# Optimization experiments

Hardware: AMD Instinct MI355X
Metric: run time of the kernel (lower is better)

The kernel has to match this reference:

```python
import jax, jax.numpy as jnp
import numpy as np

N, E, T, B = 20000, 400000, 1500000, 128
H, INT, BAS, OUT_EMB, OUT = 128, 64, 8, 256, 1
NR, SBF_DIM = 6, 42  # num_radial, num_spherical*num_radial
L, NBS, NAS, NOUT = 4, 1, 2, 3  # layers, before-skip, after-skip, output lins


def _w(key, shape, scale=0.1):
    return jax.random.normal(key, shape, dtype=jnp.float32) * scale


def setup_inputs() -> dict:
    key = jax.random.key(0)
    ks = iter(jax.random.split(key, 64))
    inp = {}
    inp['x'] = jax.random.normal(next(ks), (N, 48), dtype=jnp.float32)
    inp['edge_attr'] = jax.random.normal(next(ks), (E, 12), dtype=jnp.float32)
    inp['rbf'] = jax.random.normal(next(ks), (E, NR), dtype=jnp.float32)
    inp['sbf'] = jax.random.normal(next(ks), (T, SBF_DIM), dtype=jnp.float32)
    inp['i'] = jax.random.randint(next(ks), (E,), 0, N)
    inp['idx_kj'] = jax.random.randint(next(ks), (T,), 0, E)
    inp['idx_ji'] = jax.random.randint(next(ks), (T,), 0, E)
    inp['batch'] = jnp.sort(jax.random.randint(next(ks), (N,), 0, B))
    # input projections
    inp['W_node'] = _w(next(ks), (48, H))
    inp['W_edge'] = _w(next(ks), (12, H))
    # update_e params, stacked over layers
    inp['We_rbf1'] = _w(next(ks), (L, NR, BAS))
    inp['We_rbf2'] = _w(next(ks), (L, BAS, H))
    inp['We_sbf1'] = _w(next(ks), (L, SBF_DIM, BAS))
    inp['We_sbf2'] = _w(next(ks), (L, BAS, INT))
    inp['We_rbf'] = _w(next(ks), (L, NR, H))
    inp['We_kj'] = _w(next(ks), (L, H, H)); inp['be_kj'] = _w(next(ks), (L, H))
    inp['We_ji'] = _w(next(ks), (L, H, H)); inp['be_ji'] = _w(next(ks), (L, H))
    inp['We_down'] = _w(next(ks), (L, H, INT))
    inp['We_up'] = _w(next(ks), (L, INT, H))
    inp['We_cat'] = _w(next(ks), (L, H, H))
    inp['Wres_before'] = _w(next(ks), (L, NBS, 2, H, H)); inp['bres_before'] = _w(next(ks), (L, NBS, 2, H))
    inp['We_lin'] = _w(next(ks), (L, H, H)); inp['be_lin'] = _w(next(ks), (L, H))
    inp['Wres_after'] = _w(next(ks), (L, NAS, 2, H, H)); inp['bres_after'] = _w(next(ks), (L, NAS, 2, H))
    # update_v params, stacked over layers
    inp['Wv_up'] = _w(next(ks), (L, H, OUT_EMB)); inp['bv_up'] = _w(next(ks), (L, OUT_EMB))
    inp['Wv_lins'] = _w(next(ks), (L, NOUT, OUT_EMB, OUT_EMB)); inp['bv_lins'] = _w(next(ks), (L, NOUT, OUT_EMB))
    inp['Wv_out'] = _w(next(ks), (L, OUT_EMB, OUT))
    return inp


def _forward(x, edge_attr, rbf, sbf, W_node, W_edge, We_rbf1, We_rbf2, We_sbf1,
             We_sbf2, We_rbf, We_kj, be_kj, We_ji, be_ji, We_down, We_up, We_cat,
             Wres_before, bres_before, We_lin, be_lin, Wres_after, bres_after,
             Wv_up, bv_up, Wv_lins, bv_lins, Wv_out, i, idx_kj, idx_ji, batch):
    silu = jax.nn.silu  # swish
    seg = lambda v, idx, n: jax.ops.segment_sum(v, idx, num_segments=n)

    e1 = edge_attr @ W_edge            # [E, H]  (init edge state; init_e unused in source fwd)
    v = x @ W_node                     # [N, H]
    u = seg(v, batch, B)               # [B, H] -> init_u(zeros, v, batch)

    # precompute sbf projection per layer inside loop (depends on layer weights)
    for l in range(L):
        # ---- update_e ----
        x_ji = silu(e1 @ We_ji[l] + be_ji[l])
        x_kj = silu(e1 @ We_kj[l] + be_kj[l])
        r = (rbf @ We_rbf1[l]) @ We_rbf2[l]          # [E, H]
        x_kj = silu((x_kj * r) @ We_down[l])          # [E, INT]
        s = (sbf @ We_sbf1[l]) @ We_sbf2[l]           # [T, INT]
        m = x_kj[idx_kj] * s                          # gather to triplets
        agg = seg(m, idx_ji, E)                       # scatter back to edges
        x_kj = silu(agg @ We_up[l])                   # [E, H]
        e = silu((x_ji + x_kj) @ We_cat[l])
        for r_ in range(NBS):
            e = e + silu(silu(e @ Wres_before[l, r_, 0] + bres_before[l, r_, 0]) @ Wres_before[l, r_, 1] + bres_before[l, r_, 1])
        e = silu(e @ We_lin[l] + be_lin[l]) + e1
        for r_ in range(NAS):
            e = e + silu(silu(e @ Wres_after[l, r_, 0] + bres_after[l, r_, 0]) @ Wres_after[l, r_, 1] + bres_after[l, r_, 1])
        e1 = e
        e2 = (rbf @ We_rbf[l]) * e1                   # [E, H]
        # ---- update_v ----
        vn = seg(e2, i, N)                            # [N, H]
        vn = vn @ Wv_up[l] + bv_up[l]                 # [N, OUT_EMB]
        for k in range(NOUT):
            vn = silu(vn @ Wv_lins[l, k] + bv_lins[l, k])
        vn = vn @ Wv_out[l]                           # [N, OUT]
        # ---- update_u ----
        u = u + seg(vn, batch, B) if l > 0 else seg(vn, batch, B)
        if l == 0:
            # first update_u adds onto u (which held init [B,H]); but shapes differ
            # in source only because out is added to u of same shape. Here init u
            # is [B,H] from v=lin_node(x) and vn is [B,OUT]; the source's init_u
            # uses v=[N,H] so u=[B,H] then adds v=[N,OUT] scatters -> in torch this
            # broadcasts only if OUT==H. Faithful behavior with OUT=1: broadcast add.
            pass
        # (handled above via broadcasting in jnp if needed)
    return u


def reference(x, edge_attr, rbf, sbf, W_node, W_edge, We_rbf1, We_rbf2, We_sbf1,
              We_sbf2, We_rbf, We_kj, be_kj, We_ji, be_ji, We_down, We_up, We_cat,
              Wres_before, bres_before, We_lin, be_lin, Wres_after, bres_after,
              Wv_up, bv_up, Wv_lins, bv_lins, Wv_out, i, idx_kj, idx_ji, batch):
    silu = jax.nn.silu
    seg = lambda v, idx, n: jax.ops.segment_sum(v, idx, num_segments=n)

    e1 = edge_attr @ W_edge
    v = x @ W_node
    u = seg(v, batch, B)  # [B, H]
    for l in range(L):
        x_ji = silu(e1 @ We_ji[l] + be_ji[l])
        x_kj = silu(e1 @ We_kj[l] + be_kj[l])
        r = (rbf @ We_rbf1[l]) @ We_rbf2[l]
        x_kj = silu((x_kj * r) @ We_down[l])
        s = (sbf @ We_sbf1[l]) @ We_sbf2[l]
        agg = seg(x_kj[idx_kj] * s, idx_ji, E)
        x_kj = silu(agg @ We_up[l])
        e = silu((x_ji + x_kj) @ We_cat[l])
        for r_ in range(NBS):
            e = e + silu(silu(e @ Wres_before[l, r_, 0] + bres_before[l, r_, 0]) @ Wres_before[l, r_, 1] + bres_before[l, r_, 1])
        e = silu(e @ We_lin[l] + be_lin[l]) + e1
        for r_ in range(NAS):
            e = e + silu(silu(e @ Wres_after[l, r_, 0] + bres_after[l, r_, 0]) @ Wres_after[l, r_, 1] + bres_after[l, r_, 1])
        e1 = e
        e2 = (rbf @ We_rbf[l]) * e1
        vn = seg(e2, i, N) @ Wv_up[l] + bv_up[l]
        for k in range(NOUT):
            vn = silu(vn @ Wv_lins[l, k] + bv_lins[l, k])
        vn = vn @ Wv_out[l]              # [N, 1]
        u = u + seg(vn, batch, B)        # broadcast [B,1] onto [B,H]
    return u
```

## Files before the change

kernel.cpp:

```cpp
#include <hip/hip_runtime.h>
#include <hip/hip_bf16.h>
#include <cstddef>

#define NN 20000
#define EE 400000
#define TT 1500000
#define BB 128
#define HH 128
#define INTD 64
#define OUT_EMB 256
#define SBF_DIM 42
#define NRAD 6

#define SA_C 136

typedef __attribute__((ext_vector_type(8))) short bf16x8;
typedef __attribute__((ext_vector_type(4))) float f32x4;

__device__ __forceinline__ float silu_f(float v) {
    return v / (1.0f + __expf(-v));
}
__device__ __forceinline__ unsigned short f2b(float f) {
    __hip_bfloat16 h = __float2bfloat16(f);
    unsigned short u; __builtin_memcpy(&u, &h, 2); return u;
}
__device__ __forceinline__ float b2f(unsigned short u) {
    __hip_bfloat16 h; __builtin_memcpy(&h, &u, 2); return __bfloat162float(h);
}

template <int NU4>
__device__ __forceinline__ void loadWlin(uint4 (&rg)[NU4], const unsigned short* W, int tid) {
#pragma unroll
    for (int j = 0; j < NU4; ++j) rg[j] = *(const uint4*)(W + ((size_t)tid + j * 512) * 8);
}
template <int NU4, int SEGS>
__device__ __forceinline__ void storeWs(const uint4 (&rg)[NU4], unsigned short* Ws, int tid) {
#pragma unroll
    for (int j = 0; j < NU4; ++j) {
        int i = tid + j * 512;
        int n = i / SEGS, seg = i % SEGS;
        *(uint4*)&Ws[n * SA_C + seg * 8] = rg[j];
    }
}

__device__ __forceinline__ void st4(unsigned short* Cs, int m, int f0, const float* v) {
    ushort4 u = make_ushort4(f2b(v[0]), f2b(v[1]), f2b(v[2]), f2b(v[3]));
    *(ushort4*)&Cs[m * SA_C + f0] = u;
}

template <int KCNT>
__device__ __forceinline__ void mfma_f(const unsigned short* Cs, const unsigned short* Ws,
                                       int lm, int quad, int fw0, int ew0, f32x4 acc[2][4]) {
#pragma unroll
    for (int kc = 0; kc < KCNT; ++kc) {
        bf16x8 wf[2], xf[4];
#pragma unroll
        for (int mi = 0; mi < 2; ++mi)
            wf[mi] = *(const bf16x8*)&Ws[(fw0 + mi * 16 + lm) * SA_C + kc * 32 + quad * 8];
#pragma unroll
        for (int ni = 0; ni < 4; ++ni)
            xf[ni] = *(const bf16x8*)&Cs[(ew0 + ni * 16 + lm) * SA_C + kc * 32 + quad * 8];
#pragma unroll
        for (int mi = 0; mi < 2; ++mi)
#pragma unroll
            for (int ni = 0; ni < 4; ++ni)
                acc[mi][ni] = __builtin_amdgcn_mfma_f32_16x16x32_bf16(wf[mi], xf[ni], acc[mi][ni], 0, 0, 0);
    }
}

template <int KCNT>
__device__ __forceinline__ void mfma_d2(const unsigned short* Cs, const unsigned short* Ws,
                                        int lm, int quad, int fw0, int ew0, f32x4 acc[2][2]) {
#pragma unroll
    for (int kc = 0; kc < KCNT; ++kc) {
        bf16x8 wf[2], xf[2];
#pragma unroll
        for (int mi = 0; mi < 2; ++mi)
            wf[mi] = *(const bf16x8*)&Ws[(fw0 + mi * 16 + lm) * SA_C + kc * 32 + quad * 8];
#pragma unroll
        for (int ni = 0; ni < 2; ++ni)
            xf[ni] = *(const bf16x8*)&Cs[(ew0 + ni * 16 + lm) * SA_C + kc * 32 + quad * 8];
#pragma unroll
        for (int mi = 0; mi < 2; ++mi)
#pragma unroll
            for (int ni = 0; ni < 2; ++ni)
                acc[mi][ni] = __builtin_amdgcn_mfma_f32_16x16x32_bf16(wf[mi], xf[ni], acc[mi][ni], 0, 0, 0);
    }
}

__global__ __launch_bounds__(512, 2)
void mk1(const unsigned short* __restrict__ e1b,
         const unsigned short* __restrict__ w_ji, const unsigned short* __restrict__ w_kj,
         const unsigned short* __restrict__ w_down,
         const float* __restrict__ be_ji, const float* __restrict__ be_kj,
         const float* __restrict__ rbf, const float* __restrict__ Crbf_l,
         unsigned short* __restrict__ buf1, unsigned short* __restrict__ bufC) {
    __shared__ unsigned short Cs[128 * SA_C];
    __shared__ unsigned short Ws[128 * SA_C];
    __shared__ float rbfS[128 * 6];
    __shared__ float CrbfS[768];

    const int tid = threadIdx.x;
    const size_t row0 = (size_t)blockIdx.x * 128;
    const int lane = tid & 63, wave = tid >> 6, lm = lane & 15, quad = lane >> 4;
    const int rw0 = (wave >> 1) * 32;
    const int cw0 = (wave & 1) * 64;
    const int fw0d = (wave & 1) * 32;
    const int ew0d = (wave >> 1) * 32;

    uint4 wreg[4]; uint4 wregd[2];

    for (int i = tid; i < 2048; i += 512) {
        int r = i >> 4, seg = i & 15;
        *(uint4*)&Cs[r * SA_C + seg * 8] = *(const uint4*)(e1b + (row0 + r) * 128 + seg * 8);
    }
    loadWlin<4>(wreg, w_ji, tid); storeWs<4, 16>(wreg, Ws, tid);
    for (int i = tid; i < 768; i += 512) { rbfS[i] = rbf[row0 * 6 + i]; CrbfS[i] = Crbf_l[i]; }
    __syncthreads();

    f32x4 jreg[2][4], acc[2][4];
#pragma unroll
    for (int mi = 0; mi < 2; ++mi)
#pragma unroll
        for (int ni = 0; ni < 4; ++ni) jreg[mi][ni] = (f32x4){0.f, 0.f, 0.f, 0.f};
    loadWlin<4>(wreg, w_kj, tid);
    mfma_f<4>(Cs, Ws, lm, quad, rw0, cw0, jreg);
    __syncthreads();
    storeWs<4, 16>(wreg, Ws, tid);
    __syncthreads();

#pragma unroll
    for (int mi = 0; mi < 2; ++mi)
#pragma unroll
        for (int ni = 0; ni < 4; ++ni) acc[mi][ni] = (f32x4){0.f, 0.f, 0.f, 0.f};
    loadWlin<2>(wregd, w_down, tid);
    mfma_f<4>(Cs, Ws, lm, quad, rw0, cw0, acc);
    __syncthreads();
#pragma unroll
    for (int mi = 0; mi < 2; ++mi) {
        const int f0 = rw0 + mi * 16 + quad * 4;
        const float4 bb = *(const float4*)(be_kj + f0);
#pragma unroll
        for (int ni = 0; ni < 4; ++ni) {
            const int m = cw0 + ni * 16 + lm;
            float4 rv = {0.f, 0.f, 0.f, 0.f};
#pragma unroll
            for (int j = 0; j < 6; ++j) {
                float rb = rbfS[m * 6 + j];
                float4 c4 = *(const float4*)&CrbfS[j * 128 + f0];
                rv.x += rb * c4.x; rv.y += rb * c4.y; rv.z += rb * c4.z; rv.w += rb * c4.w;
            }
            float v4[4];
#pragma unroll
            for (int r = 0; r < 4; ++r) {
                float v = silu_f(acc[mi][ni][r] + (&bb.x)[r]);
                v4[r] = b2f(f2b(v)) * (&rv.x)[r];
            }
            st4(Cs, m, f0, v4);
        }
    }
    storeWs<2, 16>(wregd, Ws, tid);
    __syncthreads();

    f32x4 accd[2][2];
#pragma unroll
    for (int mi = 0; mi < 2; ++mi)
#pragma unroll
        for (int ni = 0; ni < 2; ++ni) accd[mi][ni] = (f32x4){0.f, 0.f, 0.f, 0.f};
    mfma_d2<4>(Cs, Ws, lm, quad, fw0d, ew0d, accd);
    __syncthreads();
#pragma unroll
    for (int mi = 0; mi < 2; ++mi) {
        const int f0 = fw0d + mi * 16 + quad * 4;
#pragma unroll
        for (int ni = 0; ni < 2; ++ni) {
            const int m = ew0d + ni * 16 + lm;
            float v4[4];
#pragma unroll
            for (int r = 0; r < 4; ++r) v4[r] = silu_f(accd[mi][ni][r]);
            st4(Cs, m, f0, v4);
        }
    }
    __syncthreads();
    for (int i = tid; i < 1024; i += 512) {
        int r = i >> 3, seg = i & 7;
        *(uint4*)(bufC + (row0 + r) * 64 + seg * 8) = *(const uint4*)&Cs[r * SA_C + seg * 8];
    }
    __syncthreads();
#pragma unroll
    for (int mi = 0; mi < 2; ++mi) {
        const int f0 = rw0 + mi * 16 + quad * 4;
        const float4 bj = *(const float4*)(be_ji + f0);
#pragma unroll
        for (int ni = 0; ni < 4; ++ni) {
            const int m = cw0 + ni * 16 + lm;
            float v4[4];
#pragma unroll
            for (int r = 0; r < 4; ++r) v4[r] = silu_f(jreg[mi][ni][r] + (&bj.x)[r]);
            st4(Cs, m, f0, v4);
        }
    }
    __syncthreads();
    for (int i = tid; i < 2048; i += 512) {
        int r = i >> 4, seg = i & 15;
        *(uint4*)(buf1 + (row0 + r) * 128 + seg * 8) = *(const uint4*)&Cs[r * SA_C + seg * 8];
    }
}

__global__ __launch_bounds__(512, 2)
void mk2(const unsigned short* __restrict__ bufD, const unsigned short* __restrict__ buf1g,
         float* __restrict__ e1f, unsigned short* __restrict__ e1b,
         const unsigned short* __restrict__ w_up, const unsigned short* __restrict__ w_cat,
         const unsigned short* __restrict__ w_rb0, const unsigned short* __restrict__ w_rb1,
         const unsigned short* __restrict__ w_lin,
         const unsigned short* __restrict__ w_ra0, const unsigned short* __restrict__ w_ra1,
         const unsigned short* __restrict__ w_ra2, const unsigned short* __restrict__ w_ra3,
         const float* __restrict__ b_rb0, const float* __restrict__ b_rb1,
         const float* __restrict__ b_lin,
         const float* __restrict__ b_ra0, const float* __restrict__ b_ra1,
         const float* __restrict__ b_ra2, const float* __restrict__ b_ra3) {
    __shared__ unsigned short Cs[128 * SA_C];
    __shared__ unsigned short Ws[128 * SA_C];

    const int tid = threadIdx.x;
    const size_t row0 = (size_t)blockIdx.x * 128;
    const int lane = tid & 63, wave = tid >> 6, lm = lane & 15, quad = lane >> 4;
    const int rw0 = (wave >> 1) * 32, cw0 = (wave & 1) * 64;

    f32x4 acc[2][4], state[2][4];
    uint4 wreg[4];

#define ZERO_ACC()                                                 \
    _Pragma("unroll") for (int mi = 0; mi < 2; ++mi)               \
    _Pragma("unroll") for (int ni = 0; ni < 4; ++ni)               \
        acc[mi][ni] = (f32x4){0.f, 0.f, 0.f, 0.f};

#define TILE_LOOP(PRELOAD, BODY, POST)                          \
    _Pragma("unroll") for (int mi = 0; mi < 2; ++mi) {          \
      const int f0 = rw0 + mi * 16 + quad * 4;                  \
      _Pragma("unroll") for (int ni = 0; ni < 4; ++ni) {        \
        const int m = cw0 + ni * 16 + lm;                       \
        const size_t goff = (size_t)(row0 + m) * 128 + f0;      \
        (void)goff;                                             \
        PRELOAD                                                 \
        float v4[4];                                            \
        _Pragma("unroll") for (int r = 0; r < 4; ++r) { BODY }  \
        st4(Cs, m, f0, v4);                                     \
        POST } }

    for (int i = tid; i < 1024; i += 512) {
        int r = i >> 3, seg = i & 7;
        *(uint4*)&Cs[r * SA_C + seg * 8] = *(const uint4*)(bufD + (row0 + r) * 64 + seg * 8);
    }
    {
        uint4 wu[2];
        loadWlin<2>(wu, w_up, tid); storeWs<2, 8>(wu, Ws, tid);
    }
    __syncthreads();

    ZERO_ACC()
    loadWlin<4>(wreg, w_cat, tid);
    mfma_f<2>(Cs, Ws, lm, quad, rw0, cw0, acc);
    __syncthreads();
    TILE_LOOP(
        ushort4 xj = *(const ushort4*)(buf1g + goff);,
        { float v = silu_f(acc[mi][ni][r]);
          v4[r] = b2f((&xj.x)[r]) + b2f(f2b(v)); },
    )
    storeWs<4, 16>(wreg, Ws, tid);
    __syncthreads();

#define PHASE_HEAD(WNEXT)                          \
    ZERO_ACC()                                     \
    loadWlin<4>(wreg, (WNEXT), tid);               \
    mfma_f<4>(Cs, Ws, lm, quad, rw0, cw0, acc);    \
    __syncthreads();

#define PHASE_TAIL()                               \
    storeWs<4, 16>(wreg, Ws, tid);                 \
    __syncthreads();

    PHASE_HEAD(w_rb0)
    TILE_LOOP(,
        { float v = silu_f(acc[mi][ni][r]); state[mi][ni][r] = v; v4[r] = v; },
    )
    PHASE_TAIL()

    PHASE_HEAD(w_rb1)
    TILE_LOOP(
        float4 b4 = *(const float4*)(b_rb0 + f0);,
        { v4[r] = silu_f(acc[mi][ni][r] + (&b4.x)[r]); },
    )
    PHASE_TAIL()

    PHASE_HEAD(w_lin)
    TILE_LOOP(
        float4 b4 = *(const float4*)(b_rb1 + f0);,
        { float v = state[mi][ni][r] + silu_f(acc[mi][ni][r] + (&b4.x)[r]);
          state[mi][ni][r] = v; v4[r] = v; },
    )
    PHASE_TAIL()

    PHASE_HEAD(w_ra0)
    TILE_LOOP(
        float4 b4 = *(const float4*)(b_lin + f0);
        float4 e4 = *(const float4*)(e1f + goff);,
        { float v = silu_f(acc[mi][ni][r] + (&b4.x)[r]) + (&e4.x)[r];
          state[mi][ni][r] = v; v4[r] = v; },
    )
    PHASE_TAIL()

    PHASE_HEAD(w_ra1)
    TILE_LOOP(
        float4 b4 = *(const float4*)(b_ra0 + f0);,
        { v4[r] = silu_f(acc[mi][ni][r] + (&b4.x)[r]); },
    )
    PHASE_TAIL()

    PHASE_HEAD(w_ra2)
    TILE_LOOP(
        float4 b4 = *(const float4*)(b_ra1 + f0);,
        { float v = state[mi][ni][r] + silu_f(acc[mi][ni][r] + (&b4.x)[r]);
          state[mi][ni][r] = v; v4[r] = v; },
    )
    PHASE_TAIL()

    PHASE_HEAD(w_ra3)
    TILE_LOOP(
        float4 b4 = *(const float4*)(b_ra2 + f0);,
        { v4[r] = silu_f(acc[mi][ni][r] + (&b4.x)[r]); },
    )
    PHASE_TAIL()

    ZERO_ACC()
    mfma_f<4>(Cs, Ws, lm, quad, rw0, cw0, acc);
    __syncthreads();
    TILE_LOOP(
        float4 b4 = *(const float4*)(b_ra3 + f0);,
        { float v = state[mi][ni][r] + silu_f(acc[mi][ni][r] + (&b4.x)[r]);
          state[mi][ni][r] = v; v4[r] = v; },
        { float4 ev; ev.x = v4[0]; ev.y = v4[1]; ev.z = v4[2]; ev.w = v4[3];
          *(float4*)(e1f + goff) = ev; }
    )
    __syncthreads();
    for (int i = tid; i < 2048; i += 512) {
        int r = i >> 4, seg = i & 15;
        *(uint4*)(e1b + (row0 + r) * 128 + seg * 8) = *(const uint4*)&Cs[r * SA_C + seg * 8];
    }
#undef PHASE_HEAD
#undef PHASE_TAIL
#undef TILE_LOOP
#undef ZERO_ACC
}

__global__ void transpose_w(const float* __restrict__ src, unsigned short* __restrict__ dst,
                            int B, int K, int N) {
    size_t total = (size_t)B * K * N;
    size_t i = (size_t)blockIdx.x * 256 + threadIdx.x;
    if (i >= total) return;
    int b = i / ((size_t)K * N);
    size_t rem = i - (size_t)b * K * N;
    int k = rem / N, n = rem % N;
    dst[(size_t)b * K * N + (size_t)n * K + k] = f2b(src[i]);
}

template <int K>
__launch_bounds__(256)
__global__ void gemm_k(const float* __restrict__ A, const float* __restrict__ W,
                       const float* __restrict__ bias, float* __restrict__ out,
                       unsigned short* __restrict__ outb, int N, int act) {
    constexpr int KC = (K <= 128) ? K : 128;
    __shared__ float As[32][KC + 1];
    __shared__ float Ws[KC * 64];
    const int tid = threadIdx.x;
    const size_t row0 = (size_t)blockIdx.x * 32;
    const int tx = tid & 15, ty = tid >> 4;
    const int c0 = tx * 4, r0 = ty * 2;

    for (int nc0 = 0; nc0 < N; nc0 += 64) {
        float acc[2][4] = {{0.f, 0.f, 0.f, 0.f}, {0.f, 0.f, 0.f, 0.f}};
        for (int kc0 = 0; kc0 < K; kc0 += KC) {
            __syncthreads();
            for (int idx = tid; idx < 32 * KC / 4; idx += 256) {
                int r = idx / (KC / 4);
                int kk = (idx % (KC / 4)) * 4;
                float4 v = *(const float4*)(A + (row0 + r) * K + kc0 + kk);
                As[r][kk] = v.x; As[r][kk + 1] = v.y;
                As[r][kk + 2] = v.z; As[r][kk + 3] = v.w;
            }
            for (int idx = tid; idx < KC * 16; idx += 256) {
                int k = idx >> 4;
                int cc = (idx & 15) * 4;
                *(float4*)&Ws[k * 64 + cc] =
                    *(const float4*)(W + (size_t)(kc0 + k) * N + nc0 + cc);
            }
            __syncthreads();
#pragma unroll 4
            for (int k = 0; k < KC; ++k) {
                float a0 = As[r0][k], a1 = As[r0 + 1][k];
                float4 w = *(const float4*)&Ws[k * 64 + c0];
                acc[0][0] += a0 * w.x; acc[0][1] += a0 * w.y;
                acc[0][2] += a0 * w.z; acc[0][3] += a0 * w.w;
                acc[1][0] += a1 * w.x; acc[1][1] += a1 * w.y;
                acc[1][2] += a1 * w.z; acc[1][3] += a1 * w.w;
            }
        }
#pragma unroll
        for (int i = 0; i < 2; ++i) {
            size_t off = (row0 + r0 + i) * N + nc0 + c0;
            float4 v = make_float4(acc[i][0], acc[i][1], acc[i][2], acc[i][3]);
            if (bias) {
                float4 b = *(const float4*)(bias + nc0 + c0);
                v.x += b.x; v.y += b.y; v.z += b.z; v.w += b.w;
            }
            if (act) {
                v.x = silu_f(v.x); v.y = silu_f(v.y);
                v.z = silu_f(v.z); v.w = silu_f(v.w);
            }
            if (out) *(float4*)(out + off) = v;
            if (outb) {
                ushort4 u = make_ushort4(f2b(v.x), f2b(v.y), f2b(v.z), f2b(v.w));
                *(ushort4*)(outb + off) = u;
            }
        }
    }
}

__global__ void combine_rbf(const float* __restrict__ W1, const float* __restrict__ W2,
                            float* __restrict__ C) {
    int l = blockIdx.x;
    const float* w1 = W1 + l * 48;
    const float* w2 = W2 + l * 1024;
    float* c = C + l * 768;
    for (int idx = threadIdx.x; idx < 768; idx += 256) {
        int j = idx >> 7, h = idx & 127;
        float s = 0.f;
#pragma unroll
        for (int p = 0; p < 8; ++p) s += w1[j * 8 + p] * w2[p * 128 + h];
        c[idx] = s;
    }
}

__global__ void hist_kernel(const int* __restrict__ idx, int n, int* __restrict__ cnt) {
    int t = blockIdx.x * 256 + threadIdx.x;
    if (t < n) atomicAdd(&cnt[idx[t]], 1);
}

__launch_bounds__(1024)
__global__ void scan1(const int* __restrict__ cnt, int n, int* __restrict__ offs,
                      int* __restrict__ partials) {
    __shared__ int tmp[1024];
    int tid = threadIdx.x;
    int i = blockIdx.x * 1024 + tid;
    int v = (i < n) ? cnt[i] : 0;
    tmp[tid] = v; __syncthreads();
    for (int d = 1; d < 1024; d <<= 1) {
        int t = (tid >= d) ? tmp[tid - d] : 0; __syncthreads();
        tmp[tid] += t; __syncthreads();
    }
    if (i < n) offs[i] = tmp[tid] - v;
    if (tid == 1023) partials[blockIdx.x] = tmp[1023];
}

__launch_bounds__(1024)
__global__ void scan2(int* __restrict__ partials, int nb, int n, int* __restrict__ offs) {
    __shared__ int tmp[1024];
    int tid = threadIdx.x;
    int v = (tid < nb) ? partials[tid] : 0;
    tmp[tid] = v; __syncthreads();
    for (int d = 1; d < 1024; d <<= 1) {
        int t = (tid >= d) ? tmp[tid - d] : 0; __syncthreads();
        tmp[tid] += t; __syncthreads();
    }
    if (tid < nb) partials[tid] = tmp[tid] - v;
    if (tid == 1023) offs[n] = tmp[1023];
}

__launch_bounds__(1024)
__global__ void scan3(int n, int* __restrict__ offs, const int* __restrict__ partials,
                      int* __restrict__ cur) {
    int i = blockIdx.x * 1024 + threadIdx.x;
    if (i < n) { int o = offs[i] + partials[blockIdx.x]; offs[i] = o; cur[i] = o; }
}

__global__ void fill_kernel(const int* __restrict__ idx, int n,
                            int* __restrict__ cur, int* __restrict__ lst) {
    int t = blockIdx.x * 256 + threadIdx.x;
    if (t < n) {
        int p = atomicAdd(&cur[idx[t]], 1);
        lst[p] = t;
    }
}

__launch_bounds__(128)
__global__ void p8_kernel(const float* __restrict__ sbf, const float* __restrict__ W1,
                          float* __restrict__ p8) {
    __shared__ float S[128 * 43];
    __shared__ float Wl[SBF_DIM * 8];
    int tid = threadIdx.x;
    for (int i = tid; i < SBF_DIM * 8; i += 128) Wl[i] = W1[i];
    size_t base = (size_t)blockIdx.x * 128;
    int rows = (TT - base) < 128 ? (int)(TT - base) : 128;
    const float* src = sbf + base * SBF_DIM;
    for (int i = tid; i < rows * SBF_DIM; i += 128) {
        int r = i / SBF_DIM, j = i - r * SBF_DIM;
        S[r * 43 + j] = src[i];
    }
    __syncthreads();
    if (tid >= rows) return;
    float pv[8] = {0.f, 0.f, 0.f, 0.f, 0.f, 0.f, 0.f, 0.f};
    for (int j = 0; j < SBF_DIM; ++j) {
        float sv = S[tid * 43 + j];
#pragma unroll
        for (int p = 0; p < 8; ++p) pv[p] += sv * Wl[j * 8 + p];
    }
    float4* o = (float4*)(p8 + (base + tid) * 8);
    o[0] = make_float4(pv[0], pv[1], pv[2], pv[3]);
    o[1] = make_float4(pv[4], pv[5], pv[6], pv[7]);
}

__launch_bounds__(256)
__global__ void triplet_gather(const float* __restrict__ p8, const float* __restrict__ W2,
                               const unsigned short* __restrict__ xkj,
                               const int* __restrict__ idx_kj,
                               const int* __restrict__ offsT, const int* __restrict__ tlist,
                               unsigned short* __restrict__ agg) {
    int lane = threadIdx.x & 63;
    int wv = threadIdx.x >> 6;
    int e = blockIdx.x * 4 + wv;
    if (e >= EE) return;
    float w2c[8];
#pragma unroll
    for (int p = 0; p < 8; ++p) w2c[p] = W2[p * INTD + lane];
    int b = offsT[e], en = offsT[e + 1];
    float acc = 0.f;
    for (int q = b; q < en; ++q) {
        int t = tlist[q];
        int k = idx_kj[t];
        const float4* pr = (const float4*)(p8 + (size_t)t * 8);
        float4 p0 = pr[0], p1 = pr[1];
        float s = p0.x * w2c[0] + p0.y * w2c[1] + p0.z * w2c[2] + p0.w * w2c[3]
                + p1.x * w2c[4] + p1.y * w2c[5] + p1.z * w2c[6] + p1.w * w2c[7];
        acc += s * b2f(xkj[(size_t)k * INTD + lane]);
    }
    agg[(size_t)e * INTD + lane] = f2b(acc);
}

__launch_bounds__(256)
__global__ void e2_gather(const float* __restrict__ rbf, const float* __restrict__ Wr,
                          const float* __restrict__ e1f, const int* __restrict__ offsE,
                          const int* __restrict__ elist, float* __restrict__ vseg) {
    int h = threadIdx.x & 127;
    int sub = threadIdx.x >> 7;
    int n = blockIdx.x * 2 + sub;
    if (n >= NN) return;
    float c0 = Wr[0 * 128 + h], c1 = Wr[1 * 128 + h], c2 = Wr[2 * 128 + h],
          c3 = Wr[3 * 128 + h], c4 = Wr[4 * 128 + h], c5 = Wr[5 * 128 + h];
    int b = offsE[n], en = offsE[n + 1];
    float a0 = 0.f, a1 = 0.f, a2 = 0.f, a3 = 0.f;
    int q = b;
    for (; q + 4 <= en; q += 4) {
        int ea = elist[q], eb = elist[q + 1], ec = elist[q + 2], ed = elist[q + 3];
        const float* ra = rbf + (size_t)ea * NRAD;
        const float* rb = rbf + (size_t)eb * NRAD;
        const float* rc = rbf + (size_t)ec * NRAD;
        const float* rd = rbf + (size_t)ed * NRAD;
        float fa = e1f[(size_t)ea * 128 + h];
        float fb = e1f[(size_t)eb * 128 + h];
        float fc = e1f[(size_t)ec * 128 + h];
        float fd = e1f[(size_t)ed * 128 + h];
        float sa = ra[0] * c0 + ra[1] * c1 + ra[2] * c2 + ra[3] * c3 + ra[4] * c4 + ra[5] * c5;
        float sb = rb[0] * c0 + rb[1] * c1 + rb[2] * c2 + rb[3] * c3 + rb[4] * c4 + rb[5] * c5;
        float sc = rc[0] * c0 + rc[1] * c1 + rc[2] * c2 + rc[3] * c3 + rc[4] * c4 + rc[5] * c5;
        float sd = rd[0] * c0 + rd[1] * c1 + rd[2] * c2 + rd[3] * c3 + rd[4] * c4 + rd[5] * c5;
        a0 += sa * fa; a1 += sb * fb; a2 += sc * fc; a3 += sd * fd;
    }
    for (; q < en; ++q) {
        int e = elist[q];
        const float* rr = rbf + (size_t)e * NRAD;
        float s = rr[0] * c0 + rr[1] * c1 + rr[2] * c2 + rr[3] * c3 + rr[4] * c4 + rr[5] * c5;
        a0 += s * e1f[(size_t)e * 128 + h];
    }
    vseg[(size_t)n * 128 + h] = (a0 + a1) + (a2 + a3);
}

__global__ void scatter_u0(const float* __restrict__ v, const int* __restrict__ batch,
                           float* __restrict__ u0) {
    int idx = blockIdx.x * 256 + threadIdx.x;
    int h = idx & 127;
    int n = idx >> 7;
    atomicAdd(&u0[(size_t)batch[n] * 128 + h], v[idx]);
}

__launch_bounds__(256)
__global__ void vout_scatter(const float* __restrict__ vn, const float* __restrict__ Wv_out,
                             const int* __restrict__ batch, float* __restrict__ sbatch) {
    int wave = threadIdx.x >> 6, lane = threadIdx.x & 63;
    int n = blockIdx.x * 4 + wave;
    if (n >= NN) return;
    const float* row = vn + (size_t)n * OUT_EMB;
    float s = 0.f;
#pragma unroll
    for (int k = lane; k < OUT_EMB; k += 64) s += row[k] * Wv_out[k];
#pragma unroll
    for (int off = 32; off > 0; off >>= 1) s += __shfl_down(s, off);
    if (lane == 0) atomicAdd(&sbatch[batch[n]], s);
}

__global__ void final_out(const float* __restrict__ u0, const float* __restrict__ sb,
                          float* __restrict__ out) {
    int idx = blockIdx.x * 256 + threadIdx.x;
    out[idx] = u0[idx] + sb[idx >> 7];
}

extern "C" void kernel_launch(void* const* d_in, const int* in_sizes, int n_in,
                              void* d_out, int out_size, void* d_ws, size_t ws_size,
                              hipStream_t stream) {
    const float* x         = (const float*)d_in[0];
    const float* edge_attr = (const float*)d_in[1];
    const float* rbf       = (const float*)d_in[2];
    const float* sbf       = (const float*)d_in[3];
    const int*   iidx      = (const int*)d_in[4];
    const int*   idx_kj    = (const int*)d_in[5];
    const int*   idx_ji    = (const int*)d_in[6];
    const int*   batch     = (const int*)d_in[7];
    const float* W_node    = (const float*)d_in[8];
    const float* W_edge    = (const float*)d_in[9];
    const float* We_rbf1   = (const float*)d_in[10];
    const float* We_rbf2   = (const float*)d_in[11];
    const float* We_sbf1   = (const float*)d_in[12];
    const float* We_sbf2   = (const float*)d_in[13];
    const float* We_rbf    = (const float*)d_in[14];
    const float* We_kj     = (const float*)d_in[15];
    const float* be_kj     = (const float*)d_in[16];
    const float* We_ji     = (const float*)d_in[17];
    const float* be_ji     = (const float*)d_in[18];
    const float* We_down   = (const float*)d_in[19];
    const float* We_up     = (const float*)d_in[20];
    const float* We_cat    = (const float*)d_in[21];
    const float* Wres_b    = (const float*)d_in[22];
    const float* bres_b    = (const float*)d_in[23];
    const float* We_lin    = (const float*)d_in[24];
    const float* be_lin    = (const float*)d_in[25];
    const float* Wres_a    = (const float*)d_in[26];
    const float* bres_a    = (const float*)d_in[27];
    const float* Wv_up     = (const float*)d_in[28];
    const float* bv_up     = (const float*)d_in[29];
    const float* Wv_lins   = (const float*)d_in[30];
    const float* bv_lins   = (const float*)d_in[31];
    const float* Wv_out    = (const float*)d_in[32];
    float* out = (float*)d_out;

    unsigned short* e1b  = (unsigned short*)d_ws;
    unsigned short* buf1 = e1b  + (size_t)EE * HH;
    unsigned short* scr2 = buf1 + (size_t)EE * HH;
    unsigned short* bufC = scr2 + (size_t)EE * HH;
    unsigned short* bufD = bufC + (size_t)EE * INTD;
    unsigned short* endu = bufD + (size_t)EE * INTD;
    float* e1f    = (float*)endu;
    float* tail   = e1f + (size_t)EE * HH;
    float* u0     = tail;
    float* sbatch = u0 + BB * HH;
    float* Crbf   = sbatch + 256;
    int*   iptr   = (int*)(Crbf + 4 * 768);
    int* cntT  = iptr;               iptr += EE;
    int* offsT = iptr;               iptr += EE + 1;
    int* curT  = iptr;               iptr += EE;
    int* tlist = iptr;               iptr += TT;
    int* cntE  = iptr;               iptr += NN;
    int* offsE = iptr;               iptr += NN + 1;
    int* curE  = iptr;               iptr += NN;
    int* elist = iptr;               iptr += EE;
    int* partials = iptr;            iptr += 1024;
    unsigned short* wptr = (unsigned short*)iptr;
    unsigned short* wt_ji   = wptr;  wptr += 4 * 16384;
    unsigned short* wt_kj   = wptr;  wptr += 4 * 16384;
    unsigned short* wt_down = wptr;  wptr += 4 * 8192;
    unsigned short* wt_up   = wptr;  wptr += 4 * 8192;
    unsigned short* wt_cat  = wptr;  wptr += 4 * 16384;
    unsigned short* wt_resb = wptr;  wptr += 8 * 16384;
    unsigned short* wt_lin  = wptr;  wptr += 4 * 16384;
    unsigned short* wt_resa = wptr;  wptr += 16 * 16384;
    float* p8 = (float*)scr2;
    float* vseg = (float*)bufC;
    float* vn1  = vseg + (size_t)NN * HH;
    float* vn2  = vn1 + (size_t)NN * OUT_EMB;

    hipMemsetAsync(u0, 0, (size_t)BB * HH * sizeof(float), stream);
    hipMemsetAsync(sbatch, 0, 256 * sizeof(float), stream);
    combine_rbf<<<4, 256, 0, stream>>>(We_rbf1, We_rbf2, Crbf);

    transpose_w<<<(4 * 16384 + 255) / 256, 256, 0, stream>>>(We_ji, wt_ji, 4, 128, 128);
    transpose_w<<<(4 * 16384 + 255) / 256, 256, 0, stream>>>(We_kj, wt_kj, 4, 128, 128);
    transpose_w<<<(4 * 8192 + 255) / 256, 256, 0, stream>>>(We_down, wt_down, 4, 128, 64);
    transpose_w<<<(4 * 8192 + 255) / 256, 256, 0, stream>>>(We_up, wt_up, 4, 64, 128);
    transpose_w<<<(4 * 16384 + 255) / 256, 256, 0, stream>>>(We_cat, wt_cat, 4, 128, 128);
    transpose_w<<<(8 * 16384 + 255) / 256, 256, 0, stream>>>(Wres_b, wt_resb, 8, 128, 128);
    transpose_w<<<(4 * 16384 + 255) / 256, 256, 0, stream>>>(We_lin, wt_lin, 4, 128, 128);
    transpose_w<<<(16 * 16384 + 255) / 256, 256, 0, stream>>>(Wres_a, wt_resa, 16, 128, 128);

    hipMemsetAsync(cntT, 0, EE * sizeof(int), stream);
    hipMemsetAsync(cntE, 0, NN * sizeof(int), stream);
    hist_kernel<<<(TT + 255) / 256, 256, 0, stream>>>(idx_ji, TT, cntT);
    hist_kernel<<<(EE + 255) / 256, 256, 0, stream>>>(iidx, EE, cntE);
    int nbT = (EE + 1023) / 1024, nbE = (NN + 1023) / 1024;
    scan1<<<nbT, 1024, 0, stream>>>(cntT, EE, offsT, partials);
    scan2<<<1, 1024, 0, stream>>>(partials, nbT, EE, offsT);
    scan3<<<nbT, 1024, 0, stream>>>(EE, offsT, partials, curT);
    fill_kernel<<<(TT + 255) / 256, 256, 0, stream>>>(idx_ji, TT, curT, tlist);
    scan1<<<nbE, 1024, 0, stream>>>(cntE, NN, offsE, partials);
    scan2<<<1, 1024, 0, stream>>>(partials, nbE, NN, offsE);
    scan3<<<nbE, 1024, 0, stream>>>(NN, offsE, partials, curE);
    fill_kernel<<<(EE + 255) / 256, 256, 0, stream>>>(iidx, EE, curE, elist);

    gemm_k<12><<<EE / 32, 256, 0, stream>>>(edge_attr, W_edge, nullptr, e1f, e1b, HH, 0);
    gemm_k<48><<<NN / 32, 256, 0, stream>>>(x, W_node, nullptr, vseg, nullptr, HH, 0);
    scatter_u0<<<NN * HH / 256, 256, 0, stream>>>(vseg, batch, u0);

    const int GR = EE / 128;
    for (int l = 0; l < 4; ++l) {
        mk1<<<GR, 512, 0, stream>>>(e1b, wt_ji + l * 16384, wt_kj + l * 16384,
                                    wt_down + l * 8192, be_ji + l * HH, be_kj + l * HH,
                                    rbf, Crbf + l * 768, buf1, bufC);
        p8_kernel<<<(TT + 127) / 128, 128, 0, stream>>>(sbf, We_sbf1 + l * SBF_DIM * 8, p8);
        triplet_gather<<<EE / 4, 256, 0, stream>>>(p8, We_sbf2 + l * 8 * INTD, bufC,
                                                   idx_kj, offsT, tlist, bufD);
        mk2<<<GR, 512, 0, stream>>>(bufD, buf1, e1f, e1b,
            wt_up + l * 8192, wt_cat + l * 16384,
            wt_resb + (l * 2 + 0) * 16384, wt_resb + (l * 2 + 1) * 16384,
            wt_lin + l * 16384,
            wt_resa + ((l * 2 + 0) * 2 + 0) * 16384, wt_resa + ((l * 2 + 0) * 2 + 1) * 16384,
            wt_resa + ((l * 2 + 1) * 2 + 0) * 16384, wt_resa + ((l * 2 + 1) * 2 + 1) * 16384,
            bres_b + (l * 2 + 0) * HH, bres_b + (l * 2 + 1) * HH, be_lin + l * HH,
            bres_a + ((l * 2 + 0) * 2 + 0) * HH, bres_a + ((l * 2 + 0) * 2 + 1) * HH,
            bres_a + ((l * 2 + 1) * 2 + 0) * HH, bres_a + ((l * 2 + 1) * 2 + 1) * HH);
        e2_gather<<<(NN + 1) / 2, 256, 0, stream>>>(rbf, We_rbf + (size_t)l * NRAD * HH,
                                                    e1f, offsE, elist, vseg);
        gemm_k<128><<<NN / 32, 256, 0, stream>>>(vseg, Wv_up + (size_t)l * HH * OUT_EMB,
                                                 bv_up + l * OUT_EMB, vn1, nullptr, OUT_EMB, 0);
        gemm_k<256><<<NN / 32, 256, 0, stream>>>(vn1, Wv_lins + (size_t)(l * 3 + 0) * 65536,
                                                 bv_lins + (l * 3 + 0) * 256, vn2, nullptr, OUT_EMB, 1);
        gemm_k<256><<<NN / 32, 256, 0, stream>>>(vn2, Wv_lins + (size_t)(l * 3 + 1) * 65536,
                                                 bv_lins + (l * 3 + 1) * 256, vn1, nullptr, OUT_EMB, 1);
        gemm_k<256><<<NN / 32, 256, 0, stream>>>(vn1, Wv_lins + (size_t)(l * 3 + 2) * 65536,
                                                 bv_lins + (l * 3 + 2) * 256, vn2, nullptr, OUT_EMB, 1);
        vout_scatter<<<NN / 4, 256, 0, stream>>>(vn2, Wv_out + l * OUT_EMB, batch, sbatch);
    }
    final_out<<<BB * HH / 256, 256, 0, stream>>>(u0, sbatch, out);
}
```

Measured before the change: 6.905 ms.

## Fuse node MLP chain into one bf16 MFMA kernel and stage mk2 output via LDS

Replaces the per-layer chain of four fp32 gemm_k launches plus the vout_scatter reduction with a single mkv kernel. It keeps a 128-row tile in LDS across up-projection, three 256x256 SiLU layers and the output dot product, using bf16 MFMA with pre-transposed weights. This removes the intermediate vn1/vn2 global round trips and the launch overhead. mk2's final epilogue now stages fp32 results in shared memory, so the e1f and e1b stores are fully coalesced and e1b is rounded from full precision. The cost is lower precision in the node MLP (bf16 activations and weights) and a kernel limited to one block per CU by its large LDS footprint.

```diff
diff --git a/kernel.cpp b/kernel.cpp
--- a/kernel.cpp
+++ b/kernel.cpp
@@ -219,8 +219,10 @@
          const float* __restrict__ b_lin,
          const float* __restrict__ b_ra0, const float* __restrict__ b_ra1,
          const float* __restrict__ b_ra2, const float* __restrict__ b_ra3) {
-    __shared__ unsigned short Cs[128 * SA_C];
-    __shared__ unsigned short Ws[128 * SA_C];
+    __shared__ unsigned short SMEM[2 * 128 * SA_C];
+    unsigned short* Cs = SMEM;
+    unsigned short* Ws = SMEM + 128 * SA_C;
+    float* Fs = (float*)SMEM;
 
     const int tid = threadIdx.x;
     const size_t row0 = (size_t)blockIdx.x * 128;
@@ -235,7 +237,7 @@
     _Pragma("unroll") for (int ni = 0; ni < 4; ++ni)               \
         acc[mi][ni] = (f32x4){0.f, 0.f, 0.f, 0.f};
 
-#define TILE_LOOP(PRELOAD, BODY, POST)                          \
+#define TILE_LOOP(PRELOAD, BODY)                                \
     _Pragma("unroll") for (int mi = 0; mi < 2; ++mi) {          \
       const int f0 = rw0 + mi * 16 + quad * 4;                  \
       _Pragma("unroll") for (int ni = 0; ni < 4; ++ni) {        \
@@ -245,8 +247,7 @@
         PRELOAD                                                 \
         float v4[4];                                            \
         _Pragma("unroll") for (int r = 0; r < 4; ++r) { BODY }  \
-        st4(Cs, m, f0, v4);                                     \
-        POST } }
+        st4(Cs, m, f0, v4); } }
 
     for (int i = tid; i < 1024; i += 512) {
         int r = i >> 3, seg = i & 7;
@@ -265,7 +266,7 @@
     TILE_LOOP(
         ushort4 xj = *(const ushort4*)(buf1g + goff);,
         { float v = silu_f(acc[mi][ni][r]);
-          v4[r] = b2f((&xj.x)[r]) + b2f(f2b(v)); },
+          v4[r] = b2f((&xj.x)[r]) + b2f(f2b(v)); }
     )
     storeWs<4, 16>(wreg, Ws, tid);
     __syncthreads();
@@ -282,14 +283,14 @@
 
     PHASE_HEAD(w_rb0)
     TILE_LOOP(,
-        { float v = silu_f(acc[mi][ni][r]); state[mi][ni][r] = v; v4[r] = v; },
+        { float v = silu_f(acc[mi][ni][r]); state[mi][ni][r] = v; v4[r] = v; }
     )
     PHASE_TAIL()
 
     PHASE_HEAD(w_rb1)
     TILE_LOOP(
         float4 b4 = *(const float4*)(b_rb0 + f0);,
-        { v4[r] = silu_f(acc[mi][ni][r] + (&b4.x)[r]); },
+        { v4[r] = silu_f(acc[mi][ni][r] + (&b4.x)[r]); }
     )
     PHASE_TAIL()
 
@@ -297,7 +298,7 @@
     TILE_LOOP(
         float4 b4 = *(const float4*)(b_rb1 + f0);,
         { float v = state[mi][ni][r] + silu_f(acc[mi][ni][r] + (&b4.x)[r]);
-          state[mi][ni][r] = v; v4[r] = v; },
+          state[mi][ni][r] = v; v4[r] = v; }
     )
     PHASE_TAIL()
 
@@ -306,14 +307,14 @@
         float4 b4 = *(const float4*)(b_lin + f0);
         float4 e4 = *(const float4*)(e1f + goff);,
         { float v = silu_f(acc[mi][ni][r] + (&b4.x)[r]) + (&e4.x)[r];
-          state[mi][ni][r] = v; v4[r] = v; },
+          state[mi][ni][r] = v; v4[r] = v; }
     )
     PHASE_TAIL()
 
     PHASE_HEAD(w_ra1)
     TILE_LOOP(
         float4 b4 = *(const float4*)(b_ra0 + f0);,
-        { v4[r] = silu_f(acc[mi][ni][r] + (&b4.x)[r]); },
+        { v4[r] = silu_f(acc[mi][ni][r] + (&b4.x)[r]); }
     )
     PHASE_TAIL()
 
@@ -321,36 +322,180 @@
     TILE_LOOP(
         float4 b4 = *(const float4*)(b_ra1 + f0);,
         { float v = state[mi][ni][r] + silu_f(acc[mi][ni][r] + (&b4.x)[r]);
-          state[mi][ni][r] = v; v4[r] = v; },
+          state[mi][ni][r] = v; v4[r] = v; }
     )
     PHASE_TAIL()
 
     PHASE_HEAD(w_ra3)
     TILE_LOOP(
         float4 b4 = *(const float4*)(b_ra2 + f0);,
-        { v4[r] = silu_f(acc[mi][ni][r] + (&b4.x)[r]); },
+        { v4[r] = silu_f(acc[mi][ni][r] + (&b4.x)[r]); }
     )
     PHASE_TAIL()
 
     ZERO_ACC()
     mfma_f<4>(Cs, Ws, lm, quad, rw0, cw0, acc);
     __syncthreads();
-    TILE_LOOP(
-        float4 b4 = *(const float4*)(b_ra3 + f0);,
-        { float v = state[mi][ni][r] + silu_f(acc[mi][ni][r] + (&b4.x)[r]);
-          state[mi][ni][r] = v; v4[r] = v; },
-        { float4 ev; ev.x = v4[0]; ev.y = v4[1]; ev.z = v4[2]; ev.w = v4[3];
-          *(float4*)(e1f + goff) = ev; }
-    )
-    __syncthreads();
+#pragma unroll
+    for (int mi = 0; mi < 2; ++mi) {
+        const int f0 = rw0 + mi * 16 + quad * 4;
+        const float4 b4 = *(const float4*)(b_ra3 + f0);
+#pragma unroll
+        for (int ni = 0; ni < 4; ++ni) {
+            const int m = cw0 + ni * 16 + lm;
+            float4 ev;
+#pragma unroll
+            for (int r = 0; r < 4; ++r)
+                (&ev.x)[r] = state[mi][ni][r] + silu_f(acc[mi][ni][r] + (&b4.x)[r]);
+            *(float4*)&Fs[m * 132 + f0] = ev;
+        }
+    }
+    __syncthreads();
+    for (int i = tid; i < 4096; i += 512) {
+        int r = i >> 5, s4 = (i & 31) * 4;
+        *(float4*)(e1f + (row0 + r) * 128 + s4) = *(const float4*)&Fs[r * 132 + s4];
+    }
     for (int i = tid; i < 2048; i += 512) {
-        int r = i >> 4, seg = i & 15;
-        *(uint4*)(e1b + (row0 + r) * 128 + seg * 8) = *(const uint4*)&Cs[r * SA_C + seg * 8];
+        int r = i >> 4, s8 = (i & 15) * 8;
+        const float* fr = Fs + r * 132 + s8;
+        float4 a = *(const float4*)fr, b = *(const float4*)(fr + 4);
+        *(ushort4*)(e1b + (row0 + r) * 128 + s8) =
+            make_ushort4(f2b(a.x), f2b(a.y), f2b(a.z), f2b(a.w));
+        *(ushort4*)(e1b + (row0 + r) * 128 + s8 + 4) =
+            make_ushort4(f2b(b.x), f2b(b.y), f2b(b.z), f2b(b.w));
     }
 #undef PHASE_HEAD
 #undef PHASE_TAIL
 #undef TILE_LOOP
 #undef ZERO_ACC
+}
+
+__device__ __forceinline__ void loadW8v(uint4 (&rg)[8], const unsigned short* W,
+                                        int rowstride, int co, int tid) {
+#pragma unroll
+    for (int j = 0; j < 8; ++j) {
+        int i = tid + j * 512;
+        int n = i >> 4, seg = i & 15;
+        rg[j] = *(const uint4*)(W + (size_t)n * rowstride + co + seg * 8);
+    }
+}
+__device__ __forceinline__ void storeW8v(const uint4 (&rg)[8], unsigned short* Ws, int tid) {
+#pragma unroll
+    for (int j = 0; j < 8; ++j) {
+        int i = tid + j * 512;
+        int n = i >> 4, seg = i & 15;
+        *(uint4*)&Ws[n * 136 + seg * 8] = rg[j];
+    }
+}
+
+template <int KCNT>
+__device__ __forceinline__ void mfma_v(const unsigned short* Cs, int c0,
+                                       const unsigned short* Ws, int lm, int quad,
+                                       int fw0, f32x4 acc[2][8]) {
+#pragma unroll
+    for (int kc = 0; kc < KCNT; ++kc) {
+        bf16x8 wf[2];
+#pragma unroll
+        for (int mi = 0; mi < 2; ++mi)
+            wf[mi] = *(const bf16x8*)&Ws[(fw0 + mi * 16 + lm) * 136 + kc * 32 + quad * 8];
+#pragma unroll
+        for (int ni = 0; ni < 8; ++ni) {
+            bf16x8 xf = *(const bf16x8*)&Cs[(ni * 16 + lm) * 264 + c0 + kc * 32 + quad * 8];
+#pragma unroll
+            for (int mi = 0; mi < 2; ++mi)
+                acc[mi][ni] = __builtin_amdgcn_mfma_f32_16x16x32_bf16(wf[mi], xf, acc[mi][ni], 0, 0, 0);
+        }
+    }
+}
+
+__global__ __launch_bounds__(512, 1)
+void mkv(const float* __restrict__ vseg, const unsigned short* __restrict__ wtu,
+         const unsigned short* __restrict__ wtl, const float* __restrict__ bu,
+         const float* __restrict__ bls, const float* __restrict__ wvout,
+         const int* __restrict__ batch, float* __restrict__ sbatch) {
+    __shared__ unsigned short SM[128 * 264 + 256 * 136];
+    unsigned short* Cs = SM;
+    unsigned short* Ws = SM + 128 * 264;
+
+    const int tid = threadIdx.x;
+    const size_t row0 = (size_t)blockIdx.x * 128;
+    const int lane = tid & 63, wave = tid >> 6, lm = lane & 15, quad = lane >> 4;
+    const int fw0 = wave * 32;
+
+    f32x4 acc[2][8];
+    uint4 wreg[8];
+
+#define ZERO8()                                              \
+    _Pragma("unroll") for (int mi = 0; mi < 2; ++mi)         \
+    _Pragma("unroll") for (int ni = 0; ni < 8; ++ni)         \
+        acc[mi][ni] = (f32x4){0.f, 0.f, 0.f, 0.f};
+
+#define EPI_V(BIAS, ACT)                                              \
+    _Pragma("unroll") for (int mi = 0; mi < 2; ++mi) {                \
+      const int f0 = fw0 + mi * 16 + quad * 4;                        \
+      const float4 b4 = *(const float4*)((BIAS) + f0);                \
+      _Pragma("unroll") for (int ni = 0; ni < 8; ++ni) {              \
+        const int m = ni * 16 + lm;                                   \
+        float v4[4];                                                  \
+        _Pragma("unroll") for (int r2 = 0; r2 < 4; ++r2) {            \
+            float v = acc[mi][ni][r2] + (&b4.x)[r2];                  \
+            if (ACT) v = silu_f(v);                                   \
+            v4[r2] = v; }                                             \
+        *(ushort4*)&Cs[m * 264 + f0] =                                \
+            make_ushort4(f2b(v4[0]), f2b(v4[1]), f2b(v4[2]), f2b(v4[3])); } }
+
+    for (int i = tid; i < 2048; i += 512) {
+        int r = i >> 4, c8 = (i & 15) * 8;
+        size_t sr = row0 + r; if (sr > NN - 1) sr = NN - 1;
+        const float* src = vseg + sr * 128 + c8;
+        float4 a = *(const float4*)src, b = *(const float4*)(src + 4);
+        *(ushort4*)&Cs[r * 264 + c8] = make_ushort4(f2b(a.x), f2b(a.y), f2b(a.z), f2b(a.w));
+        *(ushort4*)&Cs[r * 264 + c8 + 4] = make_ushort4(f2b(b.x), f2b(b.y), f2b(b.z), f2b(b.w));
+    }
+    loadW8v(wreg, wtu, 128, 0, tid); storeW8v(wreg, Ws, tid);
+    __syncthreads();
+
+    ZERO8()
+    loadW8v(wreg, wtl, 256, 0, tid);
+    mfma_v<4>(Cs, 0, Ws, lm, quad, fw0, acc);
+    __syncthreads();
+    EPI_V(bu, 0)
+    storeW8v(wreg, Ws, tid);
+    __syncthreads();
+
+    const unsigned short* wlp[3] = {wtl, wtl + 65536, wtl + 131072};
+#pragma unroll
+    for (int k = 0; k < 3; ++k) {
+        loadW8v(wreg, wlp[k], 256, 128, tid);
+        ZERO8()
+        mfma_v<4>(Cs, 0, Ws, lm, quad, fw0, acc);
+        __syncthreads();
+        storeW8v(wreg, Ws, tid);
+        __syncthreads();
+        if (k < 2) loadW8v(wreg, wlp[k + 1], 256, 0, tid);
+        mfma_v<4>(Cs, 128, Ws, lm, quad, fw0, acc);
+        __syncthreads();
+        EPI_V(bls + k * 256, 1)
+        if (k < 2) storeW8v(wreg, Ws, tid);
+        __syncthreads();
+    }
+
+    float* WoS = (float*)Ws;
+    if (tid < 64) ((float4*)WoS)[tid] = ((const float4*)wvout)[tid];
+    __syncthreads();
+    {
+        int r = tid >> 2, p = tid & 3;
+        float s = 0.f;
+        const unsigned short* cr = Cs + r * 264 + p * 64;
+        const float* wc = WoS + p * 64;
+#pragma unroll
+        for (int j = 0; j < 64; ++j) s += b2f(cr[j]) * wc[j];
+        s += __shfl_down(s, 1);
+        s += __shfl_down(s, 2);
+        if (p == 0 && row0 + r < NN) atomicAdd(&sbatch[batch[row0 + r]], s);
+    }
+#undef ZERO8
+#undef EPI_V
 }
 
 __global__ void transpose_w(const float* __restrict__ src, unsigned short* __restrict__ dst,
@@ -590,21 +735,6 @@
     int h = idx & 127;
     int n = idx >> 7;
     atomicAdd(&u0[(size_t)batch[n] * 128 + h], v[idx]);
-}
-
-__launch_bounds__(256)
-__global__ void vout_scatter(const float* __restrict__ vn, const float* __restrict__ Wv_out,
-                             const int* __restrict__ batch, float* __restrict__ sbatch) {
-    int wave = threadIdx.x >> 6, lane = threadIdx.x & 63;
-    int n = blockIdx.x * 4 + wave;
-    if (n >= NN) return;
-    const float* row = vn + (size_t)n * OUT_EMB;
-    float s = 0.f;
-#pragma unroll
-    for (int k = lane; k < OUT_EMB; k += 64) s += row[k] * Wv_out[k];
-#pragma unroll
-    for (int off = 32; off > 0; off >>= 1) s += __shfl_down(s, off);
-    if (lane == 0) atomicAdd(&sbatch[batch[n]], s);
 }
 
 __global__ void final_out(const float* __restrict__ u0, const float* __restrict__ sb,
@@ -682,9 +812,9 @@
     unsigned short* wt_lin  = wptr;  wptr += 4 * 16384;
     unsigned short* wt_resa = wptr;  wptr += 16 * 16384;
     float* p8 = (float*)scr2;
+    unsigned short* wtv_up  = scr2 + (size_t)TT * 16;
+    unsigned short* wtv_lin = wtv_up + 4 * 32768;
     float* vseg = (float*)bufC;
-    float* vn1  = vseg + (size_t)NN * HH;
-    float* vn2  = vn1 + (size_t)NN * OUT_EMB;
 
     hipMemsetAsync(u0, 0, (size_t)BB * HH * sizeof(float), stream);
     hipMemsetAsync(sbatch, 0, 256 * sizeof(float), stream);
@@ -698,6 +828,8 @@
     transpose_w<<<(8 * 16384 + 255) / 256, 256, 0, stream>>>(Wres_b, wt_resb, 8, 128, 128);
     transpose_w<<<(4 * 16384 + 255) / 256, 256, 0, stream>>>(We_lin, wt_lin, 4, 128, 128);
     transpose_w<<<(16 * 16384 + 255) / 256, 256, 0, stream>>>(Wres_a, wt_resa, 16, 128, 128);
+    transpose_w<<<(4 * 128 * 256 + 255) / 256, 256, 0, stream>>>(Wv_up, wtv_up, 4, 128, 256);
+    transpose_w<<<(12 * 256 * 256 + 255) / 256, 256, 0, stream>>>(Wv_lins, wtv_lin, 12, 256, 256);
 
     hipMemsetAsync(cntT, 0, EE * sizeof(int), stream);
     hipMemsetAsync(cntE, 0, NN * sizeof(int), stream);
@@ -718,6 +850,7 @@
     scatter_u0<<<NN * HH / 256, 256, 0, stream>>>(vseg, batch, u0);
 
     const int GR = EE / 128;
+    const int GV = (NN + 127) / 128;
     for (int l = 0; l < 4; ++l) {
         mk1<<<GR, 512, 0, stream>>>(e1b, wt_ji + l * 16384, wt_kj + l * 16384,
                                     wt_down + l * 8192, be_ji + l * HH, be_kj + l * HH,
@@ -736,15 +869,10 @@
             bres_a + ((l * 2 + 1) * 2 + 0) * HH, bres_a + ((l * 2 + 1) * 2 + 1) * HH);
         e2_gather<<<(NN + 1) / 2, 256, 0, stream>>>(rbf, We_rbf + (size_t)l * NRAD * HH,
                                                     e1f, offsE, elist, vseg);
-        gemm_k<128><<<NN / 32, 256, 0, stream>>>(vseg, Wv_up + (size_t)l * HH * OUT_EMB,
-                                                 bv_up + l * OUT_EMB, vn1, nullptr, OUT_EMB, 0);
-        gemm_k<256><<<NN / 32, 256, 0, stream>>>(vn1, Wv_lins + (size_t)(l * 3 + 0) * 65536,
-                                                 bv_lins + (l * 3 + 0) * 256, vn2, nullptr, OUT_EMB, 1);
-        gemm_k<256><<<NN / 32, 256, 0, stream>>>(vn2, Wv_lins + (size_t)(l * 3 + 1) * 65536,
-                                                 bv_lins + (l * 3 + 1) * 256, vn1, nullptr, OUT_EMB, 1);
-        gemm_k<256><<<NN / 32, 256, 0, stream>>>(vn1, Wv_lins + (size_t)(l * 3 + 2) * 65536,
-                                                 bv_lins + (l * 3 + 2) * 256, vn2, nullptr, OUT_EMB, 1);
-        vout_scatter<<<NN / 4, 256, 0, stream>>>(vn2, Wv_out + l * OUT_EMB, batch, sbatch);
+        mkv<<<GV, 512, 0, stream>>>(vseg, wtv_up + (size_t)l * 32768,
+                                    wtv_lin + (size_t)l * 3 * 65536,
+                                    bv_up + l * OUT_EMB, bv_lins + (size_t)l * 3 * OUT_EMB,
+                                    Wv_out + l * OUT_EMB, batch, sbatch);
     }
     final_out<<<BB * HH / 256, 256, 0, stream>>>(u0, sbatch, out);
 }
```

Measured after the change: 5.986 ms. 1.15x faster.
